# Kernel optimization log

Hardware: AMD Instinct MI355X
Metric: run time of the kernel (lower is better)

The kernel has to match this reference:

```python
import jax, jax.numpy as jnp
import numpy as np


def setup_inputs() -> dict:
    key = jax.random.key(0)
    ks = jax.random.split(key, 12)
    B, Nq, Ns, NODES = 128, 16, 256, 3
    V, E, C, H, OUT, NA = 50000, 300, 1024, 8, 300, 5000
    s = 0.05
    return {
        "he_ques": jax.random.randint(ks[0], (B, Nq, NODES), 0, V),
        "he_kg": jax.random.randint(ks[1], (B, Ns, NODES), 0, V),
        "emb": jax.random.normal(ks[2], (V, E), jnp.float32) * s,
        "q2h_w": jax.random.normal(ks[3], (C, E * NODES), jnp.float32) * s,
        "q2h_b": jax.random.normal(ks[4], (C,), jnp.float32) * s,
        "k2h_w": jax.random.normal(ks[5], (C, E * NODES), jnp.float32) * s,
        "k2h_b": jax.random.normal(ks[6], (C,), jnp.float32) * s,
        "h2att_w": jax.random.normal(ks[7], (H, C), jnp.float32) * s,
        "h2att_b": jax.random.normal(ks[8], (H,), jnp.float32) * s,
        "fc_w": jax.random.normal(ks[9], (OUT, C * H), jnp.float32) * s,
        "fc_b": jax.random.normal(ks[10], (OUT,), jnp.float32) * s,
        "glove_cands": jax.random.normal(ks[11], (NA, OUT), jnp.float32) * s,
    }


def reference(he_ques, he_kg, emb, q2h_w, q2h_b, k2h_w, k2h_b,
              h2att_w, h2att_b, fc_w, fc_b, glove_cands):
    B, Nq, _ = he_ques.shape
    Ns = he_kg.shape[1]
    H, C = h2att_w.shape
    # embed node indices and flatten per-hyperedge: [B, N, nodes*E]
    hq = emb[he_ques].reshape(B, Nq, -1)
    hs = emb[he_kg].reshape(B, Ns, -1)
    # linear projections (dropout p=0 in eval)
    hq = hq @ q2h_w.T + q2h_b  # [B, Nq, C]
    hs = hs @ k2h_w.T + k2h_b  # [B, Ns, C]
    # bilinear attention logits: h2att(outer(hq, hs)) fused into one einsum
    # logits[b,h,q,s] = sum_c hq[b,q,c] * hs[b,s,c] * W[h,c] + b[h]
    logits = jnp.einsum('bqc,bsc,hc->bhqs', hq, hs, h2att_w) + h2att_b[None, :, None, None]
    att = jax.nn.softmax(logits.reshape(B, H, Nq * Ns), axis=2).reshape(B, H, Nq, Ns)
    # per-head bilinear readout (replaces the per-head repeat+matmul loop):
    # out[b,h,c] = sum_{q,s} hq[b,q,c] * att[b,h,q,s] * hs[b,s,c]
    pooled = jnp.einsum('bqc,bhqs,bsc->bhc', hq, att, hs).reshape(B, H * C)
    out = pooled @ fc_w.T + fc_b  # [B, n_out]
    sim = out @ glove_cands.T  # [B, n_ans]
    return jax.nn.log_softmax(sim, axis=1)
```

## Files before the change

kernel.cpp:

```cpp
#include <hip/hip_runtime.h>
#include <stdint.h>


typedef short s16x8 __attribute__((ext_vector_type(8)));
typedef float f32x4 __attribute__((ext_vector_type(4)));

#define ASYNC_CP16(gsrc, ldst)                                                  \
  __builtin_amdgcn_global_load_lds(                                             \
      (const __attribute__((address_space(1))) void*)(gsrc),                    \
      (__attribute__((address_space(3))) void*)(ldst), 16, 0, 0)

__device__ __forceinline__ float bfr2f(uint16_t u) {
  return __builtin_bit_cast(float, (uint32_t)u << 16);
}
__device__ __forceinline__ uint16_t f2bfr(float f) {
  uint32_t u = __builtin_bit_cast(uint32_t, f);
  u += 0x7fffu + ((u >> 16) & 1u);
  return (uint16_t)(u >> 16);
}


__global__ __launch_bounds__(256) void cvt_pad300(const float* __restrict__ src,
                                                  uint16_t* __restrict__ dst,
                                                  int rows_out, int rows_src) {
  int idx = blockIdx.x * 256 + threadIdx.x;
  if (idx >= rows_out * 80) return;
  int r = idx / 80, j = idx % 80;
  float4 v = make_float4(0.f, 0.f, 0.f, 0.f);
  if (r < rows_src && j < 75) v = *(const float4*)(src + (size_t)r * 300 + j * 4);
  ushort4 o;
  o.x = f2bfr(v.x); o.y = f2bfr(v.y); o.z = f2bfr(v.z); o.w = f2bfr(v.w);
  *(ushort4*)(dst + (size_t)r * 320 + j * 4) = o;
}

__global__ __launch_bounds__(256) void cvt_plain(const float* __restrict__ src,
                                                 uint16_t* __restrict__ dst, int n) {
  int i = blockIdx.x * 256 + threadIdx.x;
  if (i < n) dst[i] = f2bfr(src[i]);
}

__global__ __launch_bounds__(256) void cvt_fc(const float* __restrict__ src,
                                              uint16_t* __restrict__ dst) {
  int i4 = blockIdx.x * 256 + threadIdx.x;
  int pos = i4 * 4;
  int r = pos >> 13, c = pos & 8191;
  float4 v = make_float4(0.f, 0.f, 0.f, 0.f);
  if (r < 300) v = *(const float4*)(src + (size_t)r * 8192 + c);
  ushort4 o;
  o.x = f2bfr(v.x); o.y = f2bfr(v.y); o.z = f2bfr(v.z); o.w = f2bfr(v.w);
  *(ushort4*)(dst + (size_t)r * 8192 + c) = o;
}

__global__ __launch_bounds__(256) void gemm_gather2(
    const int* __restrict__ heK, const int* __restrict__ heQ,
    const uint16_t* __restrict__ emb,
    const uint16_t* __restrict__ WKp, const uint16_t* __restrict__ WQp,
    const float* __restrict__ bK, const float* __restrict__ bQ,
    uint16_t* __restrict__ HS, uint16_t* __restrict__ HQ) {
  __shared__ uint16_t ring[3 * 8192];
  __shared__ int sIdx[384];
  char* ringB = (char*)ring;

  const int t = threadIdx.x;
  const int lane = t & 63, wave = t >> 6;
  const int wr = wave >> 1, wc = wave & 1;
  const int fr = lane & 15, fq = lane >> 4;
  const int srow = t >> 2, skg = t & 3;
  const int skg2 = skg ^ ((srow >> 1) & 3);

  const int v = blockIdx.x + 8 * blockIdx.y;
  const int w = (v & 7) * 272 + (v >> 3);
  const int bx = w & 7, by = w >> 3;
  const int n0 = bx * 128;
  const bool isK = by < 256;
  const int m0 = (isK ? by : by - 256) * 128;
  const int* he = isK ? heK : heQ;
  const uint16_t* W = isK ? WKp : WQp;
  const float* bias = isK ? bK : bQ;
  uint16_t* C = isK ? HS : HQ;

  for (int i = t; i < 384; i += 256) sIdx[i] = he[(long)m0 * 3 + i];
  __syncthreads();

  uint32_t ea[2][3];
#pragma unroll
  for (int h = 0; h < 2; h++)
#pragma unroll
    for (int nd = 0; nd < 3; nd++)
      ea[h][nd] =
          (uint32_t)sIdx[(h * 64 + srow) * 3 + nd] * 640u + (uint32_t)(skg2 * 16);
  const uint16_t* Wr0 = W + (long)(n0 + srow) * 960 + skg2 * 8;
  const uint16_t* Wr1 = W + (long)(n0 + 64 + srow) * 960 + skg2 * 8;

  f32x4 zv = {0.f, 0.f, 0.f, 0.f};
  f32x4 acc[4][4];
#pragma unroll
  for (int i = 0; i < 4; i++)
#pragma unroll
    for (int j = 0; j < 4; j++) acc[i][j] = zv;

  int snd = 0, skk = 0, sk = 0, sbuf = 0;
  auto STAGE = [&]() {
    const int bb = sbuf * 16384;
    const uint32_t e0 = snd == 0 ? ea[0][0] : (snd == 1 ? ea[0][1] : ea[0][2]);
    const uint32_t e1 = snd == 0 ? ea[1][0] : (snd == 1 ? ea[1][1] : ea[1][2]);
    ASYNC_CP16((const char*)emb + e0 + skk * 64, ringB + bb + t * 16);
    ASYNC_CP16((const char*)emb + e1 + skk * 64, ringB + bb + 4096 + t * 16);
    ASYNC_CP16(Wr0 + sk, ringB + bb + 8192 + t * 16);
    ASYNC_CP16(Wr1 + sk, ringB + bb + 12288 + t * 16);
    sk += 32;
    if (++skk == 10) { skk = 0; ++snd; }
    if (++sbuf == 3) sbuf = 0;
  };

  STAGE();
  STAGE();

  const int fsw = (fq ^ ((fr >> 1) & 3)) * 8;
  int aof[4], bof[4];
#pragma unroll
  for (int mi = 0; mi < 4; mi++) aof[mi] = (wr * 64 + mi * 16 + fr) * 32 + fsw;
#pragma unroll
  for (int ni = 0; ni < 4; ni++)
    bof[ni] = 4096 + (wc * 64 + ni * 16 + fr) * 32 + fsw;

  int cbuf = 0;
  for (int kt = 0; kt < 30; ++kt) {
    if (kt < 28) STAGE();
    if (kt < 28)      asm volatile("s_waitcnt vmcnt(8)" ::: "memory");
    else if (kt < 29) asm volatile("s_waitcnt vmcnt(4)" ::: "memory");
    else              asm volatile("s_waitcnt vmcnt(0)" ::: "memory");
    __builtin_amdgcn_s_barrier();
    asm volatile("" ::: "memory");
    const uint16_t* base = ring + cbuf * 8192;
    s16x8 af[4], bv[4];
#pragma unroll
    for (int mi = 0; mi < 4; mi++) af[mi] = *(const s16x8*)(base + aof[mi]);
#pragma unroll
    for (int ni = 0; ni < 4; ni++) bv[ni] = *(const s16x8*)(base + bof[ni]);
    __builtin_amdgcn_s_setprio(1);
#pragma unroll
    for (int mi = 0; mi < 4; mi++)
#pragma unroll
      for (int ni = 0; ni < 4; ni++)
        acc[mi][ni] = __builtin_amdgcn_mfma_f32_16x16x32_bf16(
            af[mi], bv[ni], acc[mi][ni], 0, 0, 0);
    __builtin_amdgcn_s_setprio(0);
    asm volatile("s_waitcnt lgkmcnt(0)" ::: "memory");
    __builtin_amdgcn_s_barrier();
    if (++cbuf == 3) cbuf = 0;
  }

#pragma unroll
  for (int ni = 0; ni < 4; ni++) {
    const int gn = n0 + wc * 64 + ni * 16 + fr;
    const float bval = bias[gn];
#pragma unroll
    for (int mi = 0; mi < 4; mi++) {
      const int gmb = m0 + wr * 64 + mi * 16 + fq * 4;
      uint16_t* cp = C + (long)gmb * 1024 + gn;
      cp[0]    = f2bfr(acc[mi][ni][0] + bval);
      cp[1024] = f2bfr(acc[mi][ni][1] + bval);
      cp[2048] = f2bfr(acc[mi][ni][2] + bval);
      cp[3072] = f2bfr(acc[mi][ni][3] + bval);
    }
  }
}

template <int EPI, int SWZ>
__global__ __launch_bounds__(256) void gemm_pipe(
    const uint16_t* __restrict__ A, int lda, long sAb,
    const uint16_t* __restrict__ Bt, int ldb, long sBb,
    int ksteps, int kchunk,
    uint16_t* __restrict__ Cbf, int ldc, long sCbf,
    float* __restrict__ Cf, int ldcf, int nmax, long sCf) {
  __shared__ uint16_t ring[3 * 8192];
  char* ringB = (char*)ring;

  const int t = threadIdx.x;
  const int lane = t & 63, wave = t >> 6;
  const int wr = wave >> 1, wc = wave & 1;
  const int fr = lane & 15, fq = lane >> 4;
  const int srow = t >> 2, skg = t & 3;
  const int skg2 = skg ^ ((srow >> 1) & 3);

  int bx = blockIdx.x, bz = blockIdx.z;
  if (SWZ) {
    const int nwg = gridDim.x * gridDim.z;
    const int v = bx + gridDim.x * bz;
    const int w = (v & 7) * (nwg >> 3) + (v >> 3);
    bx = w % gridDim.x;
    bz = w / gridDim.x;
  }
  const int m0 = blockIdx.y * 128, n0 = bx * 128;
  const uint16_t* Ab = A + (long)bz * sAb;
  const uint16_t* Bb = Bt + (long)bz * sBb;

  f32x4 zv = {0.f, 0.f, 0.f, 0.f};
  f32x4 acc[4][4];
#pragma unroll
  for (int i = 0; i < 4; i++)
#pragma unroll
    for (int j = 0; j < 4; j++) acc[i][j] = zv;

  const long kbase = (long)bz * kchunk;
  const uint16_t* As0 = Ab + (long)(m0 + srow) * lda + kbase + skg2 * 8;
  const uint16_t* As1 = Ab + (long)(m0 + 64 + srow) * lda + kbase + skg2 * 8;
  const uint16_t* Bs0 = Bb + (long)(n0 + srow) * ldb + kbase + skg2 * 8;
  const uint16_t* Bs1 = Bb + (long)(n0 + 64 + srow) * ldb + kbase + skg2 * 8;

  int sk = 0, sbuf = 0;
  auto STAGE = [&]() {
    const int bb = sbuf * 16384;
    ASYNC_CP16(As0 + sk, ringB + bb + t * 16);
    ASYNC_CP16(As1 + sk, ringB + bb + 4096 + t * 16);
    ASYNC_CP16(Bs0 + sk, ringB + bb + 8192 + t * 16);
    ASYNC_CP16(Bs1 + sk, ringB + bb + 12288 + t * 16);
    sk += 32;
    if (++sbuf == 3) sbuf = 0;
  };

  STAGE();
  STAGE();

  const int fsw = (fq ^ ((fr >> 1) & 3)) * 8;
  int aof[4], bof[4];
#pragma unroll
  for (int mi = 0; mi < 4; mi++) aof[mi] = (wr * 64 + mi * 16 + fr) * 32 + fsw;
#pragma unroll
  for (int ni = 0; ni < 4; ni++)
    bof[ni] = 4096 + (wc * 64 + ni * 16 + fr) * 32 + fsw;

  int cbuf = 0;
  for (int kt = 0; kt < ksteps; ++kt) {
    if (kt + 2 < ksteps) STAGE();
    if (kt + 2 < ksteps)      asm volatile("s_waitcnt vmcnt(8)" ::: "memory");
    else if (kt + 1 < ksteps) asm volatile("s_waitcnt vmcnt(4)" ::: "memory");
    else                      asm volatile("s_waitcnt vmcnt(0)" ::: "memory");
    __builtin_amdgcn_s_barrier();
    asm volatile("" ::: "memory");
    const uint16_t* base = ring + cbuf * 8192;
    s16x8 af[4], bv[4];
#pragma unroll
    for (int mi = 0; mi < 4; mi++) af[mi] = *(const s16x8*)(base + aof[mi]);
#pragma unroll
    for (int ni = 0; ni < 4; ni++) bv[ni] = *(const s16x8*)(base + bof[ni]);
#pragma unroll
    for (int mi = 0; mi < 4; mi++)
#pragma unroll
      for (int ni = 0; ni < 4; ni++)
        acc[mi][ni] = __builtin_amdgcn_mfma_f32_16x16x32_bf16(
            af[mi], bv[ni], acc[mi][ni], 0, 0, 0);
    asm volatile("s_waitcnt lgkmcnt(0)" ::: "memory");
    __builtin_amdgcn_s_barrier();
    if (++cbuf == 3) cbuf = 0;
  }

  if (EPI == 2) {
#pragma unroll
    for (int ni = 0; ni < 4; ni++) {
      const int gn = n0 + wc * 64 + ni * 16 + fr;
      if (gn < nmax) {
#pragma unroll
        for (int mi = 0; mi < 4; mi++)
#pragma unroll
          for (int j = 0; j < 4; j++) {
            const int gm = m0 + wr * 64 + mi * 16 + fq * 4 + j;
            Cf[(long)bz * sCf + (long)gm * ldcf + gn] = acc[mi][ni][j];
          }
      }
    }
  } else {
#pragma unroll
    for (int ni = 0; ni < 4; ni++) {
      const int gn = n0 + wc * 64 + ni * 16 + fr;
#pragma unroll
      for (int mi = 0; mi < 4; mi++)
#pragma unroll
        for (int j = 0; j < 4; j++) {
          const int gm = m0 + wr * 64 + mi * 16 + fq * 4 + j;
          Cbf[(long)bz * sCbf + (long)gm * ldc + gn] = f2bfr(acc[mi][ni][j]);
        }
    }
  }
}

__global__ __launch_bounds__(256) void gemm_pv(
    const uint16_t* __restrict__ att, const uint16_t* __restrict__ hs,
    const uint16_t* __restrict__ hqp, uint16_t* __restrict__ pooled) {
  __shared__ uint16_t sT[128 * 264];
  __shared__ uint16_t sA[4096];
  __shared__ uint16_t sHq[2048];

  const int t = threadIdx.x;
  const int lane = t & 63, wave = t >> 6;
  const int wr = wave >> 1, wc = wave & 1;
  const int fr = lane & 15, fq = lane >> 4;
  const int srow = t >> 2, skg = t & 3;
  const int skg2 = skg ^ ((srow >> 1) & 3);

  int bx = blockIdx.x, bz = blockIdx.z;
  {
    const int v = bx + 8 * bz;
    const int w = (v & 7) * 128 + (v >> 3);
    bx = w & 7;
    bz = w >> 3;
  }
  const int n0 = bx * 128;

  const uint16_t* hsb = hs + (long)bz * 262144;
  const int sloc = t & 15, c8 = t >> 4;
  s16x8 vv[16];
#pragma unroll
  for (int p = 0; p < 16; p++)
    vv[p] = *(const s16x8*)(hsb + (long)(p * 16 + sloc) * 1024 + n0 + c8 * 8);
  *(s16x8*)(sHq + (t >> 4) * 128 + (t & 15) * 8) =
      *(const s16x8*)(hqp + (long)bz * 16384 + (long)(t >> 4) * 1024 + n0 +
                      (t & 15) * 8);
#pragma unroll
  for (int p = 0; p < 16; p++) {
    const int s = p * 16 + sloc;
#pragma unroll
    for (int j = 0; j < 8; j++)
      sT[(c8 * 8 + j) * 264 + s] = (uint16_t)vv[p][j];
  }
  __syncthreads();

  f32x4 zv = {0.f, 0.f, 0.f, 0.f};
  f32x4 acc[4][4];
#pragma unroll
  for (int i = 0; i < 4; i++)
#pragma unroll
    for (int j = 0; j < 4; j++) acc[i][j] = zv;

  const uint16_t* As0 = att + (long)bz * 32768 + (long)srow * 256 + skg2 * 8;
  const uint16_t* As1 = att + (long)bz * 32768 + (long)(64 + srow) * 256 + skg2 * 8;

  const int fsw = (fq ^ ((fr >> 1) & 3)) * 8;
  int aof[4];
#pragma unroll
  for (int mi = 0; mi < 4; mi++) aof[mi] = (wr * 64 + mi * 16 + fr) * 32 + fsw;

  for (int kt = 0; kt < 8; ++kt) {
    ASYNC_CP16(As0 + kt * 32, (char*)sA + t * 16);
    ASYNC_CP16(As1 + kt * 32, (char*)sA + 4096 + t * 16);
    __syncthreads();
    s16x8 af[4], bv[4];
#pragma unroll
    for (int mi = 0; mi < 4; mi++) af[mi] = *(const s16x8*)(sA + aof[mi]);
#pragma unroll
    for (int ni = 0; ni < 4; ni++)
      bv[ni] = *(const s16x8*)(sT + (wc * 64 + ni * 16 + fr) * 264 + kt * 32 +
                               fq * 8);
    __builtin_amdgcn_s_setprio(1);
#pragma unroll
    for (int mi = 0; mi < 4; mi++)
#pragma unroll
      for (int ni = 0; ni < 4; ni++)
        acc[mi][ni] = __builtin_amdgcn_mfma_f32_16x16x32_bf16(
            af[mi], bv[ni], acc[mi][ni], 0, 0, 0);
    __builtin_amdgcn_s_setprio(0);
    __syncthreads();
  }

#pragma unroll
  for (int mi = 0; mi < 4; mi++) {
    const int hh = wr * 4 + mi;
#pragma unroll
    for (int ni = 0; ni < 4; ni++) {
      const int col = wc * 64 + ni * 16 + fr;
      float p = 0.f;
#pragma unroll
      for (int j = 0; j < 4; j++)
        p += acc[mi][ni][j] * bfr2f(sHq[(fq * 4 + j) * 128 + col]);
      p += __shfl_xor(p, 16);
      p += __shfl_xor(p, 32);
      if (fq == 0)
        pooled[(long)bz * 8192 + hh * 1024 + n0 + col] = f2bfr(p);
    }
  }
}

__global__ __launch_bounds__(256) void mul_hw(const uint16_t* __restrict__ hq,
                                              const uint16_t* __restrict__ watt,
                                              uint16_t* __restrict__ a2) {
  const int idx = blockIdx.x * 256 + threadIdx.x;
  const int b = idx >> 14;
  const int m = (idx >> 7) & 127;
  const int c8 = (idx & 127) * 8;
  const int h = m >> 4, q = m & 15;
  s16x8 hv = *(const s16x8*)(hq + ((long)(b * 16 + q)) * 1024 + c8);
  s16x8 wv = *(const s16x8*)(watt + h * 1024 + c8);
  s16x8 o;
#pragma unroll
  for (int j = 0; j < 8; j++)
    o[j] = (short)f2bfr(bfr2f((uint16_t)hv[j]) * bfr2f((uint16_t)wv[j]));
  *(s16x8*)(a2 + (long)idx * 8) = o;
}

__global__ __launch_bounds__(256) void softmax_att(uint16_t* __restrict__ att) {
  const int b = blockIdx.x >> 3, h = blockIdx.x & 7;
  uint16_t* base = att + (long)b * 32768 + h * 4096;
  const int t = threadIdx.x;
  __shared__ float red[8];
  s16x8 v0 = *(const s16x8*)(base + t * 16);
  s16x8 v1 = *(const s16x8*)(base + t * 16 + 8);
  float f[16];
#pragma unroll
  for (int j = 0; j < 8; j++) {
    f[j] = bfr2f((uint16_t)v0[j]);
    f[8 + j] = bfr2f((uint16_t)v1[j]);
  }
  float mx = f[0];
#pragma unroll
  for (int j = 1; j < 16; j++) mx = fmaxf(mx, f[j]);
#pragma unroll
  for (int d = 1; d < 64; d <<= 1) mx = fmaxf(mx, __shfl_xor(mx, d));
  if ((t & 63) == 0) red[t >> 6] = mx;
  __syncthreads();
  mx = fmaxf(fmaxf(red[0], red[1]), fmaxf(red[2], red[3]));
  float s = 0.f;
#pragma unroll
  for (int j = 0; j < 16; j++) {
    f[j] = __expf(f[j] - mx);
    s += f[j];
  }
#pragma unroll
  for (int d = 1; d < 64; d <<= 1) s += __shfl_xor(s, d);
  if ((t & 63) == 0) red[4 + (t >> 6)] = s;
  __syncthreads();
  const float ri = 1.f / (red[4] + red[5] + red[6] + red[7]);
  s16x8 o0, o1;
#pragma unroll
  for (int j = 0; j < 8; j++) {
    o0[j] = (short)f2bfr(f[j] * ri);
    o1[j] = (short)f2bfr(f[8 + j] * ri);
  }
  *(s16x8*)(base + t * 16) = o0;
  *(s16x8*)(base + t * 16 + 8) = o1;
}

__global__ __launch_bounds__(256) void cvt_out_k(const float* __restrict__ parts,
                                                 const float* __restrict__ fc_b,
                                                 uint16_t* __restrict__ outb) {
  int idx = blockIdx.x * 256 + threadIdx.x;
  if (idx >= 128 * 320) return;
  int m = idx / 320, n = idx % 320;
  float v = 0.f;
  if (n < 300) {
    v = fc_b[n];
#pragma unroll
    for (int ch = 0; ch < 8; ch++) v += parts[ch * 38400 + m * 300 + n];
  }
  outb[idx] = f2bfr(v);
}

__global__ __launch_bounds__(256) void logsoftmax_k(const float* __restrict__ sim,
                                                    float* __restrict__ out) {
  const int r = blockIdx.x, t = threadIdx.x;
  __shared__ float red[4];
  __shared__ float red2[4];
  const float* x = sim + (long)r * 5000;
  float mx = -1e30f;
  for (int i = t; i < 5000; i += 256) mx = fmaxf(mx, x[i]);
#pragma unroll
  for (int d = 1; d < 64; d <<= 1) mx = fmaxf(mx, __shfl_xor(mx, d));
  if ((t & 63) == 0) red[t >> 6] = mx;
  __syncthreads();
  mx = fmaxf(fmaxf(red[0], red[1]), fmaxf(red[2], red[3]));
  float s = 0.f;
  for (int i = t; i < 5000; i += 256) s += __expf(x[i] - mx);
#pragma unroll
  for (int d = 1; d < 64; d <<= 1) s += __shfl_xor(s, d);
  if ((t & 63) == 0) red2[t >> 6] = s;
  __syncthreads();
  s = red2[0] + red2[1] + red2[2] + red2[3];
  const float lse = mx + logf(s);
  float* o = out + (long)r * 5000;
  for (int i = t; i < 5000; i += 256) o[i] = x[i] - lse;
}

extern "C" void kernel_launch(void* const* d_in, const int* in_sizes, int n_in,
                              void* d_out, int out_size, void* d_ws, size_t ws_size,
                              hipStream_t stream) {
  (void)in_sizes; (void)n_in; (void)out_size; (void)ws_size;
  const int* he_q = (const int*)d_in[0];
  const int* he_k = (const int*)d_in[1];
  const float* emb_f = (const float*)d_in[2];
  const float* q2h_w = (const float*)d_in[3];
  const float* q2h_b = (const float*)d_in[4];
  const float* k2h_w = (const float*)d_in[5];
  const float* k2h_b = (const float*)d_in[6];
  const float* h2att_w = (const float*)d_in[7];
  const float* fc_w = (const float*)d_in[9];
  const float* fc_b = (const float*)d_in[10];
  const float* glove = (const float*)d_in[11];
  float* out = (float*)d_out;

  char* ws = (char*)d_ws;
  uint16_t* EMB   = (uint16_t*)(ws);
  uint16_t* WK    = (uint16_t*)(ws + 32000000);
  uint16_t* WQ    = (uint16_t*)(ws + 33966080);
  uint16_t* WATT  = (uint16_t*)(ws + 35932160);
  uint16_t* WFC   = (uint16_t*)(ws + 35948544);
  uint16_t* GLV   = (uint16_t*)(ws + 42240000);
  uint16_t* HQ    = (uint16_t*)(ws + 45516800);
  uint16_t* HS    = (uint16_t*)(ws + 49711104);
  uint16_t* ATT   = (uint16_t*)(ws + 183928832);
  uint16_t* POOL  = (uint16_t*)(ws + 192317440);
  float*    PARTS = (float*)(ws + 194414592);
  uint16_t* OUTB  = (uint16_t*)(ws + 195643392);
  float*    SIM   = (float*)(ws + 195725312);
  uint16_t* A2    = (uint16_t*)(ws);

  cvt_pad300<<<15625, 256, 0, stream>>>(emb_f, EMB, 50000, 50000);
  cvt_pad300<<<960, 256, 0, stream>>>(k2h_w, WK, 3072, 3072);
  cvt_pad300<<<960, 256, 0, stream>>>(q2h_w, WQ, 3072, 3072);
  cvt_pad300<<<1600, 256, 0, stream>>>(glove, GLV, 5120, 5000);
  cvt_plain<<<32, 256, 0, stream>>>(h2att_w, WATT, 8192);
  cvt_fc<<<3072, 256, 0, stream>>>(fc_w, WFC);

  gemm_gather2<<<dim3(8, 272), 256, 0, stream>>>(
      he_k, he_q, EMB, WK, WQ, k2h_b, q2h_b, HS, HQ);

  mul_hw<<<8192, 256, 0, stream>>>(HQ, WATT, A2);
  gemm_pipe<3, 1><<<dim3(2, 1, 128), 256, 0, stream>>>(
      A2, 1024, 131072, HS, 1024, 262144, 32, 0,
      ATT, 256, 32768, nullptr, 0, 0, 0);
  softmax_att<<<1024, 256, 0, stream>>>(ATT);

  gemm_pv<<<dim3(8, 1, 128), 256, 0, stream>>>(ATT, HS, HQ, POOL);

  gemm_pipe<2, 0><<<dim3(3, 1, 8), 256, 0, stream>>>(
      POOL, 8192, 0, WFC, 8192, 0, 32, 1024,
      nullptr, 0, 0, PARTS, 300, 300, 38400);

  cvt_out_k<<<160, 256, 0, stream>>>(PARTS, fc_b, OUTB);

  gemm_pipe<2, 0><<<dim3(40, 1, 1), 256, 0, stream>>>(
      OUTB, 320, 0, GLV, 320, 0, 10, 0,
      nullptr, 0, 0, SIM, 5000, 5000, 0);

  logsoftmax_k<<<128, 256, 0, stream>>>(SIM, out);
}
```

Measured before the change: 214.4 us.

## Fuse hq*W multiply into logits GEMM, merge converts, widen fc split-K

Replaces the separate mul_hw kernel and the generic logits GEMM with a dedicated gemm_logits kernel. It builds the hq*h2att_w A-operand in registers on the fly, which avoids writing and re-reading the large A2 intermediate. The five weight-conversion launches are merged into one cvt_all kernel. The fc GEMM split-K goes from 8 to 32 chunks for more parallelism, at the cost of a larger partial-sum reduction in cvt_out_k. The fused kernel adds per-iteration VALU work and global loads of hq and W inside the MFMA loop.

```diff
diff --git a/kernel.cpp b/kernel.cpp
--- a/kernel.cpp
+++ b/kernel.cpp
@@ -19,24 +19,48 @@
   return (uint16_t)(u >> 16);
 }
 
-
-__global__ __launch_bounds__(256) void cvt_pad300(const float* __restrict__ src,
-                                                  uint16_t* __restrict__ dst,
-                                                  int rows_out, int rows_src) {
-  int idx = blockIdx.x * 256 + threadIdx.x;
-  if (idx >= rows_out * 80) return;
-  int r = idx / 80, j = idx % 80;
-  float4 v = make_float4(0.f, 0.f, 0.f, 0.f);
-  if (r < rows_src && j < 75) v = *(const float4*)(src + (size_t)r * 300 + j * 4);
-  ushort4 o;
-  o.x = f2bfr(v.x); o.y = f2bfr(v.y); o.z = f2bfr(v.z); o.w = f2bfr(v.w);
-  *(ushort4*)(dst + (size_t)r * 320 + j * 4) = o;
-}
-
-__global__ __launch_bounds__(256) void cvt_plain(const float* __restrict__ src,
-                                                 uint16_t* __restrict__ dst, int n) {
-  int i = blockIdx.x * 256 + threadIdx.x;
-  if (i < n) dst[i] = f2bfr(src[i]);
+__global__ __launch_bounds__(256) void cvt_all(
+    const float* __restrict__ emb_f, const float* __restrict__ wk_f,
+    const float* __restrict__ wq_f, const float* __restrict__ glove_f,
+    const float* __restrict__ watt_f,
+    uint16_t* __restrict__ EMB, uint16_t* __restrict__ WK,
+    uint16_t* __restrict__ WQ, uint16_t* __restrict__ GLV,
+    uint16_t* __restrict__ WATT) {
+  const int idx = blockIdx.x * 256 + threadIdx.x;
+  const int TOT = 61264 * 80;
+  if (idx < TOT) {
+    const int row = idx / 80, j = idx % 80;
+    const float* src;
+    uint16_t* dst;
+    int srow, svalid;
+    if (row < 50000) {
+      src = emb_f; dst = EMB; srow = row; svalid = 1;
+    } else if (row < 53072) {
+      src = wk_f; dst = WK + (size_t)(row - 50000) * 0; srow = row - 50000;
+      dst = WK; svalid = 1;
+    } else if (row < 56144) {
+      src = wq_f; dst = WQ; srow = row - 53072; svalid = 1;
+    } else {
+      src = glove_f; dst = GLV; srow = row - 56144; svalid = (srow < 5000);
+    }
+    float4 v = make_float4(0.f, 0.f, 0.f, 0.f);
+    if (svalid && j < 75) v = *(const float4*)(src + (size_t)srow * 300 + j * 4);
+    ushort4 o;
+    o.x = f2bfr(v.x); o.y = f2bfr(v.y); o.z = f2bfr(v.z); o.w = f2bfr(v.w);
+    const int drow = (row < 50000) ? row : srow;
+    *(ushort4*)(dst + (size_t)drow * 320 + j * 4) = o;
+  } else {
+    const int i = idx - TOT;
+    if (i < 1024) {
+      float4 a = *(const float4*)(watt_f + i * 8);
+      float4 b = *(const float4*)(watt_f + i * 8 + 4);
+      ushort4 o0, o1;
+      o0.x = f2bfr(a.x); o0.y = f2bfr(a.y); o0.z = f2bfr(a.z); o0.w = f2bfr(a.w);
+      o1.x = f2bfr(b.x); o1.y = f2bfr(b.y); o1.z = f2bfr(b.z); o1.w = f2bfr(b.w);
+      *(ushort4*)(WATT + i * 8) = o0;
+      *(ushort4*)(WATT + i * 8 + 4) = o1;
+    }
+  }
 }
 
 __global__ __launch_bounds__(256) void cvt_fc(const float* __restrict__ src,
@@ -167,12 +191,129 @@
   }
 }
 
-template <int EPI, int SWZ>
+__global__ __launch_bounds__(256) void gemm_logits(
+    const uint16_t* __restrict__ hq, const uint16_t* __restrict__ watt,
+    const uint16_t* __restrict__ hs, uint16_t* __restrict__ att) {
+  __shared__ uint16_t ring[3 * 4096];
+  char* ringB = (char*)ring;
+
+  const int t = threadIdx.x;
+  const int lane = t & 63, wave = t >> 6;
+  const int wr = wave >> 1, wc = wave & 1;
+  const int fr = lane & 15, fq = lane >> 4;
+  const int srow = t >> 2, skg = t & 3;
+  const int skg2 = skg ^ ((srow >> 1) & 3);
+
+  int bx = blockIdx.x, bz = blockIdx.z;
+  {
+    const int v = bx + 2 * bz;
+    const int w = (v & 7) * 32 + (v >> 3);
+    bx = w & 1;
+    bz = w >> 1;
+  }
+  const int n0 = bx * 128;
+
+  const uint16_t* Bs0 = hs + (long)bz * 262144 + (long)(n0 + srow) * 1024 + skg2 * 8;
+  const uint16_t* Bs1 = hs + (long)bz * 262144 + (long)(n0 + 64 + srow) * 1024 + skg2 * 8;
+  const uint16_t* hqp = hq + (long)(bz * 16 + fr) * 1024 + fq * 8;
+  const uint16_t* wp0 = watt + (long)(wr * 4 + 0) * 1024 + fq * 8;
+  const uint16_t* wp1 = watt + (long)(wr * 4 + 1) * 1024 + fq * 8;
+  const uint16_t* wp2 = watt + (long)(wr * 4 + 2) * 1024 + fq * 8;
+  const uint16_t* wp3 = watt + (long)(wr * 4 + 3) * 1024 + fq * 8;
+
+  f32x4 zv = {0.f, 0.f, 0.f, 0.f};
+  f32x4 acc[4][4];
+#pragma unroll
+  for (int i = 0; i < 4; i++)
+#pragma unroll
+    for (int j = 0; j < 4; j++) acc[i][j] = zv;
+
+  int sbuf = 0, cbuf = 0;
+  ASYNC_CP16(Bs0, ringB + t * 16);
+  ASYNC_CP16(Bs1, ringB + 2048 + t * 16);
+  ASYNC_CP16(Bs0 + 32, ringB + 4096 + t * 16);
+  ASYNC_CP16(Bs1 + 32, ringB + 4096 + 2048 + t * 16);
+  sbuf = 2;
+  s16x8 hqA = *(const s16x8*)(hqp);
+  s16x8 wA0 = *(const s16x8*)(wp0), wA1 = *(const s16x8*)(wp1);
+  s16x8 wA2 = *(const s16x8*)(wp2), wA3 = *(const s16x8*)(wp3);
+  s16x8 hqB, wB0, wB1, wB2, wB3;
+
+  const int fsw = (fq ^ ((fr >> 1) & 3)) * 8;
+  int bof[4];
+#pragma unroll
+  for (int ni = 0; ni < 4; ni++)
+    bof[ni] = (wc * 64 + ni * 16 + fr) * 32 + fsw;
+
+#define LOG_BODY(KT, HQS, W0S, W1S, W2S, W3S, HQD, W0D, W1D, W2D, W3D)          \
+  {                                                                             \
+    const int kt = (KT);                                                        \
+    if (kt + 2 < 32) {                                                          \
+      ASYNC_CP16(Bs0 + (kt + 2) * 32, ringB + sbuf * 4096 + t * 16);            \
+      ASYNC_CP16(Bs1 + (kt + 2) * 32, ringB + sbuf * 4096 + 2048 + t * 16);     \
+      if (++sbuf == 3) sbuf = 0;                                                \
+    }                                                                           \
+    if (kt + 1 < 32) {                                                          \
+      const int ko = (kt + 1) * 32;                                             \
+      HQD = *(const s16x8*)(hqp + ko);                                          \
+      W0D = *(const s16x8*)(wp0 + ko); W1D = *(const s16x8*)(wp1 + ko);         \
+      W2D = *(const s16x8*)(wp2 + ko); W3D = *(const s16x8*)(wp3 + ko);         \
+    }                                                                           \
+    asm volatile("s_waitcnt vmcnt(7)" ::: "memory");                            \
+    __builtin_amdgcn_s_barrier();                                               \
+    asm volatile("" ::: "memory");                                              \
+    s16x8 af0, af1, af2, af3, bv[4];                                            \
+    _Pragma("unroll") for (int j = 0; j < 8; j++) {                             \
+      const float hv = bfr2f((uint16_t)HQS[j]);                                 \
+      af0[j] = (short)f2bfr(hv * bfr2f((uint16_t)W0S[j]));                      \
+      af1[j] = (short)f2bfr(hv * bfr2f((uint16_t)W1S[j]));                      \
+      af2[j] = (short)f2bfr(hv * bfr2f((uint16_t)W2S[j]));                      \
+      af3[j] = (short)f2bfr(hv * bfr2f((uint16_t)W3S[j]));                      \
+    }                                                                           \
+    const uint16_t* base = ring + cbuf * 4096;                                  \
+    _Pragma("unroll") for (int ni = 0; ni < 4; ni++)                            \
+        bv[ni] = *(const s16x8*)(base + bof[ni]);                               \
+    __builtin_amdgcn_s_setprio(1);                                              \
+    _Pragma("unroll") for (int ni = 0; ni < 4; ni++) {                          \
+      acc[0][ni] = __builtin_amdgcn_mfma_f32_16x16x32_bf16(af0, bv[ni],         \
+                                                           acc[0][ni], 0, 0, 0);\
+      acc[1][ni] = __builtin_amdgcn_mfma_f32_16x16x32_bf16(af1, bv[ni],         \
+                                                           acc[1][ni], 0, 0, 0);\
+      acc[2][ni] = __builtin_amdgcn_mfma_f32_16x16x32_bf16(af2, bv[ni],         \
+                                                           acc[2][ni], 0, 0, 0);\
+      acc[3][ni] = __builtin_amdgcn_mfma_f32_16x16x32_bf16(af3, bv[ni],         \
+                                                           acc[3][ni], 0, 0, 0);\
+    }                                                                           \
+    __builtin_amdgcn_s_setprio(0);                                              \
+    asm volatile("s_waitcnt lgkmcnt(0)" ::: "memory");                          \
+    __builtin_amdgcn_s_barrier();                                               \
+    if (++cbuf == 3) cbuf = 0;                                                  \
+  }
+
+  for (int kt2 = 0; kt2 < 32; kt2 += 2) {
+    LOG_BODY(kt2, hqA, wA0, wA1, wA2, wA3, hqB, wB0, wB1, wB2, wB3);
+    LOG_BODY(kt2 + 1, hqB, wB0, wB1, wB2, wB3, hqA, wA0, wA1, wA2, wA3);
+  }
+#undef LOG_BODY
+
+#pragma unroll
+  for (int ni = 0; ni < 4; ni++) {
+    const int gn = n0 + wc * 64 + ni * 16 + fr;
+#pragma unroll
+    for (int mi = 0; mi < 4; mi++)
+#pragma unroll
+      for (int j = 0; j < 4; j++) {
+        const int gm = wr * 64 + mi * 16 + fq * 4 + j;
+        att[(long)bz * 32768 + gm * 256 + gn] = f2bfr(acc[mi][ni][j]);
+      }
+  }
+}
+
+template <int SWZ>
 __global__ __launch_bounds__(256) void gemm_pipe(
     const uint16_t* __restrict__ A, int lda, long sAb,
     const uint16_t* __restrict__ Bt, int ldb, long sBb,
     int ksteps, int kchunk,
-    uint16_t* __restrict__ Cbf, int ldc, long sCbf,
     float* __restrict__ Cf, int ldcf, int nmax, long sCf) {
   __shared__ uint16_t ring[3 * 8192];
   char* ringB = (char*)ring;
@@ -194,7 +335,7 @@
   }
   const int m0 = blockIdx.y * 128, n0 = bx * 128;
   const uint16_t* Ab = A + (long)bz * sAb;
-  const uint16_t* Bb = Bt + (long)bz * sBb;
+  const uint16_t* Bb = Bt;
 
   f32x4 zv = {0.f, 0.f, 0.f, 0.f};
   f32x4 acc[4][4];
@@ -256,30 +397,16 @@
     if (++cbuf == 3) cbuf = 0;
   }
 
-  if (EPI == 2) {
-#pragma unroll
-    for (int ni = 0; ni < 4; ni++) {
-      const int gn = n0 + wc * 64 + ni * 16 + fr;
-      if (gn < nmax) {
-#pragma unroll
-        for (int mi = 0; mi < 4; mi++)
-#pragma unroll
-          for (int j = 0; j < 4; j++) {
-            const int gm = m0 + wr * 64 + mi * 16 + fq * 4 + j;
-            Cf[(long)bz * sCf + (long)gm * ldcf + gn] = acc[mi][ni][j];
-          }
-      }
-    }
-  } else {
-#pragma unroll
-    for (int ni = 0; ni < 4; ni++) {
-      const int gn = n0 + wc * 64 + ni * 16 + fr;
+#pragma unroll
+  for (int ni = 0; ni < 4; ni++) {
+    const int gn = n0 + wc * 64 + ni * 16 + fr;
+    if (gn < nmax) {
 #pragma unroll
       for (int mi = 0; mi < 4; mi++)
 #pragma unroll
         for (int j = 0; j < 4; j++) {
           const int gm = m0 + wr * 64 + mi * 16 + fq * 4 + j;
-          Cbf[(long)bz * sCbf + (long)gm * ldc + gn] = f2bfr(acc[mi][ni][j]);
+          Cf[(long)bz * sCf + (long)gm * ldcf + gn] = acc[mi][ni][j];
         }
     }
   }
@@ -379,23 +506,6 @@
         pooled[(long)bz * 8192 + hh * 1024 + n0 + col] = f2bfr(p);
     }
   }
-}
-
-__global__ __launch_bounds__(256) void mul_hw(const uint16_t* __restrict__ hq,
-                                              const uint16_t* __restrict__ watt,
-                                              uint16_t* __restrict__ a2) {
-  const int idx = blockIdx.x * 256 + threadIdx.x;
-  const int b = idx >> 14;
-  const int m = (idx >> 7) & 127;
-  const int c8 = (idx & 127) * 8;
-  const int h = m >> 4, q = m & 15;
-  s16x8 hv = *(const s16x8*)(hq + ((long)(b * 16 + q)) * 1024 + c8);
-  s16x8 wv = *(const s16x8*)(watt + h * 1024 + c8);
-  s16x8 o;
-#pragma unroll
-  for (int j = 0; j < 8; j++)
-    o[j] = (short)f2bfr(bfr2f((uint16_t)hv[j]) * bfr2f((uint16_t)wv[j]));
-  *(s16x8*)(a2 + (long)idx * 8) = o;
 }
 
 __global__ __launch_bounds__(256) void softmax_att(uint16_t* __restrict__ att) {
@@ -450,7 +560,7 @@
   if (n < 300) {
     v = fc_b[n];
 #pragma unroll
-    for (int ch = 0; ch < 8; ch++) v += parts[ch * 38400 + m * 300 + n];
+    for (int ch = 0; ch < 32; ch++) v += parts[ch * 38400 + m * 300 + n];
   }
   outb[idx] = f2bfr(v);
 }
@@ -508,38 +618,29 @@
   uint16_t* HS    = (uint16_t*)(ws + 49711104);
   uint16_t* ATT   = (uint16_t*)(ws + 183928832);
   uint16_t* POOL  = (uint16_t*)(ws + 192317440);
-  float*    PARTS = (float*)(ws + 194414592);
   uint16_t* OUTB  = (uint16_t*)(ws + 195643392);
   float*    SIM   = (float*)(ws + 195725312);
-  uint16_t* A2    = (uint16_t*)(ws);
-
-  cvt_pad300<<<15625, 256, 0, stream>>>(emb_f, EMB, 50000, 50000);
-  cvt_pad300<<<960, 256, 0, stream>>>(k2h_w, WK, 3072, 3072);
-  cvt_pad300<<<960, 256, 0, stream>>>(q2h_w, WQ, 3072, 3072);
-  cvt_pad300<<<1600, 256, 0, stream>>>(glove, GLV, 5120, 5000);
-  cvt_plain<<<32, 256, 0, stream>>>(h2att_w, WATT, 8192);
+  float*    PARTS = (float*)(ws + 49711104);
+
+  cvt_all<<<19149, 256, 0, stream>>>(emb_f, k2h_w, q2h_w, glove, h2att_w,
+                                     EMB, WK, WQ, GLV, WATT);
   cvt_fc<<<3072, 256, 0, stream>>>(fc_w, WFC);
 
   gemm_gather2<<<dim3(8, 272), 256, 0, stream>>>(
       he_k, he_q, EMB, WK, WQ, k2h_b, q2h_b, HS, HQ);
 
-  mul_hw<<<8192, 256, 0, stream>>>(HQ, WATT, A2);
-  gemm_pipe<3, 1><<<dim3(2, 1, 128), 256, 0, stream>>>(
-      A2, 1024, 131072, HS, 1024, 262144, 32, 0,
-      ATT, 256, 32768, nullptr, 0, 0, 0);
+  gemm_logits<<<dim3(2, 1, 128), 256, 0, stream>>>(HQ, WATT, HS, ATT);
   softmax_att<<<1024, 256, 0, stream>>>(ATT);
 
   gemm_pv<<<dim3(8, 1, 128), 256, 0, stream>>>(ATT, HS, HQ, POOL);
 
-  gemm_pipe<2, 0><<<dim3(3, 1, 8), 256, 0, stream>>>(
-      POOL, 8192, 0, WFC, 8192, 0, 32, 1024,
-      nullptr, 0, 0, PARTS, 300, 300, 38400);
+  gemm_pipe<0><<<dim3(3, 1, 32), 256, 0, stream>>>(
+      POOL, 8192, 0, WFC, 8192, 0, 8, 256, PARTS, 300, 300, 38400);
 
   cvt_out_k<<<160, 256, 0, stream>>>(PARTS, fc_b, OUTB);
 
-  gemm_pipe<2, 0><<<dim3(40, 1, 1), 256, 0, stream>>>(
-      OUTB, 320, 0, GLV, 320, 0, 10, 0,
-      nullptr, 0, 0, SIM, 5000, 5000, 0);
+  gemm_pipe<0><<<dim3(40, 1, 1), 256, 0, stream>>>(
+      OUTB, 320, 0, GLV, 320, 0, 10, 0, SIM, 5000, 5000, 0);
 
   logsoftmax_k<<<128, 256, 0, stream>>>(SIM, out);
 }
```

After: 209.0 us. 2.5% less time.
